# Optimization experiments

Hardware: AMD Instinct MI355X
Metric: run time of the kernel (lower is better)

The kernel has to match this reference:

```python
import jax, jax.numpy as jnp
import numpy as np

N_U = 100000; N_I = 100000; E = 500000
D_U = 256; D_I = 300; H = 128


def graph_conv(x_src, src, dst, n_src, n_dst, W, b, act):
    ones = jnp.ones(src.shape[0], dtype=x_src.dtype)
    deg_out = jnp.clip(jax.ops.segment_sum(ones, src, num_segments=n_src), 1.0)
    deg_in = jnp.clip(jax.ops.segment_sum(ones, dst, num_segments=n_dst), 1.0)
    h = (x_src * jax.lax.rsqrt(deg_out)[:, None]) @ W          # [n_src, H]
    m = jax.ops.segment_sum(h[src], dst, num_segments=n_dst)   # scatter-sum over edges
    m = m * jax.lax.rsqrt(deg_in)[:, None] + b
    return jax.nn.relu(m) if act else m


def setup_inputs():
    key = jax.random.key(0)
    ks = iter(jax.random.split(key, 64))
    f32 = jnp.float32
    inp = {}
    inp['feat_user'] = jax.random.normal(next(ks), (N_U, D_U), f32)
    inp['feat_item'] = jax.random.normal(next(ks), (N_I, D_I), f32)
    for et, (ns, nd) in [('uu', (N_U, N_U)), ('ui', (N_U, N_I)), ('iu', (N_I, N_U))]:
        inp[f'src_{et}'] = jax.random.randint(next(ks), (E,), 0, ns, dtype=jnp.int32)
        inp[f'dst_{et}'] = jax.random.randint(next(ks), (E,), 0, nd, dtype=jnp.int32)
    # HeteroLinear params
    inp['We_u'] = jax.random.normal(next(ks), (D_U, H), f32) * 0.02
    inp['be_u'] = jax.random.normal(next(ks), (H,), f32) * 0.02
    inp['We_i'] = jax.random.normal(next(ks), (D_I, H), f32) * 0.02
    inp['be_i'] = jax.random.normal(next(ks), (H,), f32) * 0.02
    # per-layer per-etype GraphConv params (3 layers x 3 etypes)
    for l in range(3):
        for et in ['uu', 'ui', 'iu']:
            inp[f'W{l}_{et}'] = jax.random.normal(next(ks), (H, H), f32) * 0.02
            inp[f'b{l}_{et}'] = jax.random.normal(next(ks), (H,), f32) * 0.02
    return inp


def reference(feat_user, feat_item, src_uu, dst_uu, src_ui, dst_ui, src_iu, dst_iu,
              We_u, be_u, We_i, be_i,
              W0_uu, b0_uu, W0_ui, b0_ui, W0_iu, b0_iu,
              W1_uu, b1_uu, W1_ui, b1_ui, W1_iu, b1_iu,
              W2_uu, b2_uu, W2_ui, b2_ui, W2_iu, b2_iu):
    # HeteroLinear embed
    hu = feat_user @ We_u + be_u
    hi = feat_item @ We_i + be_i
    # layer 0 (relu inside each GraphConv, then sum-aggregate per dst ntype)
    hu2 = graph_conv(hu, src_uu, dst_uu, N_U, N_U, W0_uu, b0_uu, True) \
        + graph_conv(hi, src_iu, dst_iu, N_I, N_U, W0_iu, b0_iu, True)
    hi2 = graph_conv(hu, src_ui, dst_ui, N_U, N_I, W0_ui, b0_ui, True)
    hu, hi = hu2, hi2
    # layer 1 (hidden)
    hu2 = graph_conv(hu, src_uu, dst_uu, N_U, N_U, W1_uu, b1_uu, True) \
        + graph_conv(hi, src_iu, dst_iu, N_I, N_U, W1_iu, b1_iu, True)
    hi2 = graph_conv(hu, src_ui, dst_ui, N_U, N_I, W1_ui, b1_ui, True)
    hu, hi = hu2, hi2
    # layer 2 (no activation)
    hu2 = graph_conv(hu, src_uu, dst_uu, N_U, N_U, W2_uu, b2_uu, False) \
        + graph_conv(hi, src_iu, dst_iu, N_I, N_U, W2_iu, b2_iu, False)
    hi2 = graph_conv(hu, src_ui, dst_ui, N_U, N_I, W2_ui, b2_ui, False)
    return hu2, hi2
```

## Files before the change

kernel.cpp:

```cpp
#include <hip/hip_runtime.h>

#define NU 100000
#define NI 100000
#define NE 500000
#define HD 128

using bf16x8 = __attribute__((ext_vector_type(8))) __bf16;
using f32x4  = __attribute__((ext_vector_type(4))) float;

__global__ __launch_bounds__(256) void src_count(
    const int* __restrict__ s0, const int* __restrict__ s1,
    const int* __restrict__ s2, float* __restrict__ deg)
{
    long long t = (long long)blockIdx.x * 256 + threadIdx.x;
    if (t >= 3LL * NE) return;
    int a = (int)(t / NE);
    int e = (int)(t - (long long)a * NE);
    const int* p = (a == 0) ? s0 : (a == 1) ? s1 : s2;
    atomicAdd(&deg[a * 200000 + p[e]], 1.0f);
}

__global__ __launch_bounds__(256) void deg_finalize(float* __restrict__ deg)
{
    int t = blockIdx.x * 256 + threadIdx.x;
    if (t < 600000) deg[t] = rsqrtf(fmaxf(deg[t], 1.0f));
}

__global__ __launch_bounds__(256) void rs_from_cnt(const int* __restrict__ cnt,
                                                   float* __restrict__ rs, int n)
{
    int t = blockIdx.x * 256 + threadIdx.x;
    if (t < n) rs[t] = rsqrtf(fmaxf((float)cnt[t], 1.0f));
}

__global__ __launch_bounds__(256) void count_dst(const int* __restrict__ dst,
                                                 int* __restrict__ cnt)
{
    int e = blockIdx.x * 256 + threadIdx.x;
    if (e < NE) atomicAdd(&cnt[dst[e]], 1);
}

__global__ __launch_bounds__(256) void scan_block(const int* __restrict__ cnt, int n,
                                                  int* __restrict__ rp,
                                                  int* __restrict__ bsum)
{
    __shared__ int s[256];
    int gid = blockIdx.x * 256 + threadIdx.x;
    int v = (gid < n) ? cnt[gid] : 0;
    s[threadIdx.x] = v;
    __syncthreads();
#pragma unroll
    for (int off = 1; off < 256; off <<= 1) {
        int t = (threadIdx.x >= off) ? s[threadIdx.x - off] : 0;
        __syncthreads();
        s[threadIdx.x] += t;
        __syncthreads();
    }
    if (gid < n) rp[gid] = s[threadIdx.x] - v;
    if (threadIdx.x == 255) bsum[blockIdx.x] = s[255];
}

__global__ __launch_bounds__(512) void scan_bsums(int* __restrict__ bsum, int nb)
{
    __shared__ int s[512];
    int v = (threadIdx.x < nb) ? bsum[threadIdx.x] : 0;
    s[threadIdx.x] = v;
    __syncthreads();
#pragma unroll
    for (int off = 1; off < 512; off <<= 1) {
        int t = (threadIdx.x >= off) ? s[threadIdx.x - off] : 0;
        __syncthreads();
        s[threadIdx.x] += t;
        __syncthreads();
    }
    if (threadIdx.x < nb) bsum[threadIdx.x] = s[threadIdx.x] - v;
    if (threadIdx.x == 0) bsum[nb] = s[nb - 1];
}

__global__ __launch_bounds__(256) void scan_add(int* __restrict__ rp,
                                                const int* __restrict__ bsum,
                                                int n, int nb)
{
    int gid = blockIdx.x * 256 + threadIdx.x;
    if (gid < n) rp[gid] += bsum[blockIdx.x];
    if (gid == 0) rp[n] = bsum[nb];
}

__global__ __launch_bounds__(256) void csr_fill(const int* __restrict__ src,
                                                const int* __restrict__ dst,
                                                const int* __restrict__ rp,
                                                int* __restrict__ cursor,
                                                int* __restrict__ eidx)
{
    int e = blockIdx.x * 256 + threadIdx.x;
    if (e >= NE) return;
    int d = dst[e];
    int pos = rp[d] + atomicAdd(&cursor[d], 1);
    eidx[pos] = src[e];
}

__global__ __launch_bounds__(256) void gather_scaled(
    const float* __restrict__ x, const float* __restrict__ rs,
    const int* __restrict__ rp, const int* __restrict__ eidx,
    float* __restrict__ m, int n)
{
    int row = blockIdx.x * 8 + (threadIdx.x >> 5);
    int c = (threadIdx.x & 31) * 4;
    if (row >= n) return;
    int beg = rp[row], end = rp[row + 1];
    float ax = 0.f, ay = 0.f, az = 0.f, aw = 0.f;
    for (int p = beg; p < end; ++p) {
        int s = eidx[p];
        float sc = rs[s];
        float4 v = *(const float4*)(x + (long long)s * HD + c);
        ax = fmaf(v.x, sc, ax);
        ay = fmaf(v.y, sc, ay);
        az = fmaf(v.z, sc, az);
        aw = fmaf(v.w, sc, aw);
    }
    *(float4*)(m + (long long)row * HD + c) = make_float4(ax, ay, az, aw);
}

__global__ __launch_bounds__(256) void convert_w(
    const float* __restrict__ W, int K, int Kpad,
    __bf16* __restrict__ Wh, __bf16* __restrict__ Wl)
{
    int t = blockIdx.x * 256 + threadIdx.x;
    if (t >= 128 * Kpad) return;
    int k = t >> 7;
    int n = t & 127;
    float x = (k < K) ? W[k * 128 + n] : 0.f;
    __bf16 h = (__bf16)x;
    float r = x - (float)h;
    Wh[n * Kpad + k] = h;
    Wl[n * Kpad + k] = (__bf16)r;
}

__global__ __launch_bounds__(256) void gemm128_mfma(
    const float* __restrict__ A, int K, int Kpad, int M,
    const __bf16* __restrict__ Wh, const __bf16* __restrict__ Wl,
    const float* __restrict__ bias,
    const float* __restrict__ out_scale,
    int do_relu, int do_accum,
    float* __restrict__ C)
{
    __shared__ __bf16 sAh[64 * 40];
    __shared__ __bf16 sAl[64 * 40];
    __shared__ __bf16 sWh[128 * 40];
    __shared__ __bf16 sWl[128 * 40];

    const int tid  = threadIdx.x;
    const int row0 = blockIdx.x * 64;
    const int lane = tid & 63;
    const int wv   = tid >> 6;
    const int lr   = lane & 15;
    const int lq   = lane >> 4;

    f32x4 acc[4][2];
#pragma unroll
    for (int i = 0; i < 4; ++i)
#pragma unroll
        for (int j = 0; j < 2; ++j)
#pragma unroll
            for (int t = 0; t < 4; ++t) acc[i][j][t] = 0.f;

    const int arow  = tid >> 2;
    const int akoff = (tid & 3) << 3;
    const int wcol  = tid >> 1;
    const int wkoff = (tid & 1) << 4;

    const int nk = Kpad >> 5;
    for (int kc = 0; kc < nk; ++kc) {
        const int k0 = kc << 5;
        {
            int row = row0 + arow;
            int k = k0 + akoff;
            float f[8];
            if (row < M && k + 7 < K) {
                float4 v0 = *(const float4*)(A + (long long)row * K + k);
                float4 v1 = *(const float4*)(A + (long long)row * K + k + 4);
                f[0] = v0.x; f[1] = v0.y; f[2] = v0.z; f[3] = v0.w;
                f[4] = v1.x; f[5] = v1.y; f[6] = v1.z; f[7] = v1.w;
            } else {
#pragma unroll
                for (int t = 0; t < 8; ++t)
                    f[t] = (row < M && k + t < K) ? A[(long long)row * K + k + t] : 0.f;
            }
            bf16x8 h8, l8;
#pragma unroll
            for (int t = 0; t < 8; ++t) {
                __bf16 h = (__bf16)f[t];
                h8[t] = h;
                l8[t] = (__bf16)(f[t] - (float)h);
            }
            *(bf16x8*)(&sAh[arow * 40 + akoff]) = h8;
            *(bf16x8*)(&sAl[arow * 40 + akoff]) = l8;
        }
        {
            const __bf16* ph = Wh + (long long)wcol * Kpad + k0 + wkoff;
            const __bf16* pl = Wl + (long long)wcol * Kpad + k0 + wkoff;
            bf16x8 w0 = *(const bf16x8*)(ph);
            bf16x8 w1 = *(const bf16x8*)(ph + 8);
            bf16x8 x0 = *(const bf16x8*)(pl);
            bf16x8 x1 = *(const bf16x8*)(pl + 8);
            *(bf16x8*)(&sWh[wcol * 40 + wkoff])     = w0;
            *(bf16x8*)(&sWh[wcol * 40 + wkoff + 8]) = w1;
            *(bf16x8*)(&sWl[wcol * 40 + wkoff])     = x0;
            *(bf16x8*)(&sWl[wcol * 40 + wkoff + 8]) = x1;
        }
        __syncthreads();
        bf16x8 bh[2], bl[2];
#pragma unroll
        for (int j = 0; j < 2; ++j) {
            int c = wv * 32 + j * 16 + lr;
            bh[j] = *(const bf16x8*)(&sWh[c * 40 + lq * 8]);
            bl[j] = *(const bf16x8*)(&sWl[c * 40 + lq * 8]);
        }
#pragma unroll
        for (int i = 0; i < 4; ++i) {
            bf16x8 ah = *(const bf16x8*)(&sAh[(i * 16 + lr) * 40 + lq * 8]);
            bf16x8 al = *(const bf16x8*)(&sAl[(i * 16 + lr) * 40 + lq * 8]);
#pragma unroll
            for (int j = 0; j < 2; ++j) {
                acc[i][j] = __builtin_amdgcn_mfma_f32_16x16x32_bf16(ah, bh[j], acc[i][j], 0, 0, 0);
                acc[i][j] = __builtin_amdgcn_mfma_f32_16x16x32_bf16(ah, bl[j], acc[i][j], 0, 0, 0);
                acc[i][j] = __builtin_amdgcn_mfma_f32_16x16x32_bf16(al, bh[j], acc[i][j], 0, 0, 0);
            }
        }
        __syncthreads();
    }

#pragma unroll
    for (int j = 0; j < 2; ++j) {
        int col = wv * 32 + j * 16 + lr;
        float bv = bias ? bias[col] : 0.f;
#pragma unroll
        for (int i = 0; i < 4; ++i) {
            int r0 = row0 + i * 16 + lq * 4;
#pragma unroll
            for (int t = 0; t < 4; ++t) {
                int row = r0 + t;
                if (row < M) {
                    float s = out_scale ? out_scale[row] : 1.f;
                    float v = acc[i][j][t] * s + bv;
                    if (do_relu) v = fmaxf(v, 0.f);
                    float* cp = C + (long long)row * 128 + col;
                    if (do_accum) v += *cp;
                    *cp = v;
                }
            }
        }
    }
}

static inline void build_csr(const int* src, const int* dst, int n_dst,
                             int* cnt, int* rp, int* cursor, int* eidx,
                             int* bsum, float* rs_in, hipStream_t stream)
{
    const int nb = (n_dst + 255) / 256;
    hipMemsetAsync(cnt, 0, n_dst * sizeof(int), stream);
    count_dst<<<(NE + 255) / 256, 256, 0, stream>>>(dst, cnt);
    rs_from_cnt<<<nb, 256, 0, stream>>>(cnt, rs_in, n_dst);
    scan_block<<<nb, 256, 0, stream>>>(cnt, n_dst, rp, bsum);
    scan_bsums<<<1, 512, 0, stream>>>(bsum, nb);
    scan_add<<<nb, 256, 0, stream>>>(rp, bsum, n_dst, nb);
    hipMemsetAsync(cursor, 0, n_dst * sizeof(int), stream);
    csr_fill<<<(NE + 255) / 256, 256, 0, stream>>>(src, dst, rp, cursor, eidx);
}

extern "C" void kernel_launch(void* const* d_in, const int* in_sizes, int n_in,
                              void* d_out, int out_size, void* d_ws, size_t ws_size,
                              hipStream_t stream)
{
    const float* feat_user = (const float*)d_in[0];
    const float* feat_item = (const float*)d_in[1];
    const int* src_uu = (const int*)d_in[2];
    const int* dst_uu = (const int*)d_in[3];
    const int* src_ui = (const int*)d_in[4];
    const int* dst_ui = (const int*)d_in[5];
    const int* src_iu = (const int*)d_in[6];
    const int* dst_iu = (const int*)d_in[7];
    const float* We_u = (const float*)d_in[8];
    const float* be_u = (const float*)d_in[9];
    const float* We_i = (const float*)d_in[10];
    const float* be_i = (const float*)d_in[11];

    float* hu = (float*)d_out;
    float* hi = hu + (size_t)NU * HD;

    float* ws   = (float*)d_ws;
    float* m_uu = ws;
    float* m_ui = m_uu + (size_t)NU * HD;
    float* m_iu = m_ui + (size_t)NI * HD;
    float* deg  = m_iu + (size_t)NU * HD;
    float* rs_out_uu = deg + 0;
    float* rs_in_uu  = deg + 100000;
    float* rs_out_ui = deg + 200000;
    float* rs_in_ui  = deg + 300000;
    float* rs_out_iu = deg + 400000;
    float* rs_in_iu  = deg + 500000;

    int* ib = (int*)(deg + 600000);
    int* rp_uu   = ib;                 ib += 100001;
    int* rp_ui   = ib;                 ib += 100001;
    int* rp_iu   = ib;                 ib += 100001;
    int* ei_uu   = ib;                 ib += NE;
    int* ei_ui   = ib;                 ib += NE;
    int* ei_iu   = ib;                 ib += NE;
    int* cnt     = ib;                 ib += 100000;
    int* cursor  = ib;                 ib += 100000;
    int* bsum    = ib;                 ib += 1024;

    uintptr_t wp = ((uintptr_t)ib + 63) & ~(uintptr_t)63;
    __bf16* wtbuf = (__bf16*)wp;
    __bf16* eu_h = wtbuf;
    __bf16* eu_l = eu_h + 128 * 256;
    __bf16* ei_h = eu_l + 128 * 256;
    __bf16* ei_l = ei_h + 128 * 320;
    __bf16* lw   = ei_l + 128 * 320;

    convert_w<<<(128 * 256 + 255) / 256, 256, 0, stream>>>(We_u, 256, 256, eu_h, eu_l);
    convert_w<<<(128 * 320 + 255) / 256, 256, 0, stream>>>(We_i, 300, 320, ei_h, ei_l);
    for (int l = 0; l < 3; ++l)
        for (int e = 0; e < 3; ++e) {
            const float* W = (const float*)d_in[12 + 6 * l + 2 * e];
            __bf16* h = lw + (size_t)(l * 3 + e) * 2 * 16384;
            convert_w<<<64, 256, 0, stream>>>(W, 128, 128, h, h + 16384);
        }

    hipMemsetAsync(deg, 0, 600000 * sizeof(float), stream);
    src_count<<<(3 * NE + 255) / 256, 256, 0, stream>>>(src_uu, src_ui, src_iu, deg);
    deg_finalize<<<(600000 + 255) / 256, 256, 0, stream>>>(deg);

    build_csr(src_uu, dst_uu, NU, cnt, rp_uu, cursor, ei_uu, bsum, rs_in_uu, stream);
    build_csr(src_ui, dst_ui, NI, cnt, rp_ui, cursor, ei_ui, bsum, rs_in_ui, stream);
    build_csr(src_iu, dst_iu, NU, cnt, rp_iu, cursor, ei_iu, bsum, rs_in_iu, stream);

    gemm128_mfma<<<(NU + 63) / 64, 256, 0, stream>>>(feat_user, 256, 256, NU,
                                                     eu_h, eu_l, be_u, nullptr, 0, 0, hu);
    gemm128_mfma<<<(NI + 63) / 64, 256, 0, stream>>>(feat_item, 300, 320, NI,
                                                     ei_h, ei_l, be_i, nullptr, 0, 0, hi);

    const int gat_blocks_u = (NU + 7) / 8;
    const int gat_blocks_i = (NI + 7) / 8;
    const int gemm_blocks_u = (NU + 63) / 64;
    const int gemm_blocks_i = (NI + 63) / 64;
    for (int l = 0; l < 3; ++l) {
        const float* b_uu = (const float*)d_in[12 + 6 * l + 1];
        const float* b_ui = (const float*)d_in[12 + 6 * l + 3];
        const float* b_iu = (const float*)d_in[12 + 6 * l + 5];
        __bf16* wh_uu = lw + (size_t)(l * 3 + 0) * 2 * 16384;
        __bf16* wh_ui = lw + (size_t)(l * 3 + 1) * 2 * 16384;
        __bf16* wh_iu = lw + (size_t)(l * 3 + 2) * 2 * 16384;
        const int relu = (l < 2) ? 1 : 0;

        gather_scaled<<<gat_blocks_u, 256, 0, stream>>>(hu, rs_out_uu, rp_uu, ei_uu, m_uu, NU);
        gather_scaled<<<gat_blocks_i, 256, 0, stream>>>(hu, rs_out_ui, rp_ui, ei_ui, m_ui, NI);
        gather_scaled<<<gat_blocks_u, 256, 0, stream>>>(hi, rs_out_iu, rp_iu, ei_iu, m_iu, NU);
        gemm128_mfma<<<gemm_blocks_u, 256, 0, stream>>>(m_uu, HD, HD, NU,
            wh_uu, wh_uu + 16384, b_uu, rs_in_uu, relu, 0, hu);
        gemm128_mfma<<<gemm_blocks_u, 256, 0, stream>>>(m_iu, HD, HD, NU,
            wh_iu, wh_iu + 16384, b_iu, rs_in_iu, relu, 1, hu);
        gemm128_mfma<<<gemm_blocks_i, 256, 0, stream>>>(m_ui, HD, HD, NI,
            wh_ui, wh_ui + 16384, b_ui, rs_in_ui, relu, 0, hi);
    }
}
```

Before: 1.523 ms.

## Add K=128 GEMM with register-resident weights and double-buffered A; unroll gather

Adds a specialised GEMM for the per-layer 128x128 transforms. Each wave keeps its bf16 hi/lo weight fragments in registers, and each block walks several 32-row chunks, double-buffering the converted A tiles in shared memory. This removes the per-tile weight reload and the K-loop staging of the generic kernel, at the cost of more registers and lower grid parallelism. Separately, the gather loop is unrolled by four so more independent row loads are in flight per thread.

Result: no change. 1.526 ms (+0.2%).

```diff
diff --git a/kernel.cpp b/kernel.cpp
--- a/kernel.cpp
+++ b/kernel.cpp
@@ -109,14 +109,29 @@
     if (row >= n) return;
     int beg = rp[row], end = rp[row + 1];
     float ax = 0.f, ay = 0.f, az = 0.f, aw = 0.f;
-    for (int p = beg; p < end; ++p) {
+    int p = beg;
+    for (; p + 4 <= end; p += 4) {
+        int s0 = eidx[p], s1 = eidx[p + 1], s2 = eidx[p + 2], s3 = eidx[p + 3];
+        float r0 = rs[s0], r1 = rs[s1], r2 = rs[s2], r3 = rs[s3];
+        float4 v0 = *(const float4*)(x + (long long)s0 * HD + c);
+        float4 v1 = *(const float4*)(x + (long long)s1 * HD + c);
+        float4 v2 = *(const float4*)(x + (long long)s2 * HD + c);
+        float4 v3 = *(const float4*)(x + (long long)s3 * HD + c);
+        ax = fmaf(v0.x, r0, ax); ay = fmaf(v0.y, r0, ay);
+        az = fmaf(v0.z, r0, az); aw = fmaf(v0.w, r0, aw);
+        ax = fmaf(v1.x, r1, ax); ay = fmaf(v1.y, r1, ay);
+        az = fmaf(v1.z, r1, az); aw = fmaf(v1.w, r1, aw);
+        ax = fmaf(v2.x, r2, ax); ay = fmaf(v2.y, r2, ay);
+        az = fmaf(v2.z, r2, az); aw = fmaf(v2.w, r2, aw);
+        ax = fmaf(v3.x, r3, ax); ay = fmaf(v3.y, r3, ay);
+        az = fmaf(v3.z, r3, az); aw = fmaf(v3.w, r3, aw);
+    }
+    for (; p < end; ++p) {
         int s = eidx[p];
         float sc = rs[s];
         float4 v = *(const float4*)(x + (long long)s * HD + c);
-        ax = fmaf(v.x, sc, ax);
-        ay = fmaf(v.y, sc, ay);
-        az = fmaf(v.z, sc, az);
-        aw = fmaf(v.w, sc, aw);
+        ax = fmaf(v.x, sc, ax); ay = fmaf(v.y, sc, ay);
+        az = fmaf(v.z, sc, az); aw = fmaf(v.w, sc, aw);
     }
     *(float4*)(m + (long long)row * HD + c) = make_float4(ax, ay, az, aw);
 }
@@ -134,6 +149,142 @@
     float r = x - (float)h;
     Wh[n * Kpad + k] = h;
     Wl[n * Kpad + k] = (__bf16)r;
+}
+
+#define CPB 3
+__global__ __launch_bounds__(256) void gemm_k128(
+    const float* __restrict__ A, int M,
+    const __bf16* __restrict__ Wh, const __bf16* __restrict__ Wl,
+    const float* __restrict__ bias,
+    const float* __restrict__ out_scale,
+    int do_relu, int do_accum,
+    float* __restrict__ C)
+{
+    __shared__ __bf16 sAh[2][32 * 136];
+    __shared__ __bf16 sAl[2][32 * 136];
+
+    const int tid  = threadIdx.x;
+    const int lane = tid & 63;
+    const int wv   = tid >> 6;
+    const int lr   = lane & 15;
+    const int lq   = lane >> 4;
+
+    bf16x8 bh[2][4], bl[2][4];
+#pragma unroll
+    for (int j = 0; j < 2; ++j)
+#pragma unroll
+        for (int kc = 0; kc < 4; ++kc) {
+            int col = wv * 32 + j * 16 + lr;
+            int k = kc * 32 + lq * 8;
+            bh[j][kc] = *(const bf16x8*)(Wh + col * 128 + k);
+            bl[j][kc] = *(const bf16x8*)(Wl + col * 128 + k);
+        }
+
+    const int nch = (M + 31) >> 5;
+    const int c0 = blockIdx.x * CPB;
+    const int cend = (c0 + CPB < nch) ? c0 + CPB : nch;
+
+    const int srow  = tid >> 3;
+    const int skoff = (tid & 7) << 4;
+
+    float4 pre[4];
+
+#define LOADREG(c)                                                              \
+    {                                                                           \
+        int row = (c) * 32 + srow;                                              \
+        if (row < M) {                                                          \
+            const float* p = A + (long long)row * 128 + skoff;                  \
+            pre[0] = *(const float4*)(p);                                       \
+            pre[1] = *(const float4*)(p + 4);                                   \
+            pre[2] = *(const float4*)(p + 8);                                   \
+            pre[3] = *(const float4*)(p + 12);                                  \
+        } else {                                                                \
+            pre[0] = pre[1] = pre[2] = pre[3] = make_float4(0.f, 0.f, 0.f, 0.f);\
+        }                                                                       \
+    }
+
+#define CVTWRITE(buf)                                                           \
+    {                                                                           \
+        float fv[16] = {pre[0].x, pre[0].y, pre[0].z, pre[0].w,                 \
+                        pre[1].x, pre[1].y, pre[1].z, pre[1].w,                 \
+                        pre[2].x, pre[2].y, pre[2].z, pre[2].w,                 \
+                        pre[3].x, pre[3].y, pre[3].z, pre[3].w};                \
+        bf16x8 h0, h1, l0, l1;                                                  \
+        _Pragma("unroll")                                                       \
+        for (int t = 0; t < 8; ++t) {                                           \
+            __bf16 h = (__bf16)fv[t];                                           \
+            h0[t] = h; l0[t] = (__bf16)(fv[t] - (float)h);                      \
+        }                                                                       \
+        _Pragma("unroll")                                                       \
+        for (int t = 0; t < 8; ++t) {                                           \
+            __bf16 h = (__bf16)fv[8 + t];                                       \
+            h1[t] = h; l1[t] = (__bf16)(fv[8 + t] - (float)h);                  \
+        }                                                                       \
+        *(bf16x8*)(&sAh[buf][srow * 136 + skoff])     = h0;                     \
+        *(bf16x8*)(&sAh[buf][srow * 136 + skoff + 8]) = h1;                     \
+        *(bf16x8*)(&sAl[buf][srow * 136 + skoff])     = l0;                     \
+        *(bf16x8*)(&sAl[buf][srow * 136 + skoff + 8]) = l1;                     \
+    }
+
+    LOADREG(c0);
+    CVTWRITE(0);
+    __syncthreads();
+
+    for (int c = c0; c < cend; ++c) {
+        const int buf = (c - c0) & 1;
+        const bool more = (c + 1 < cend);
+        if (more) LOADREG(c + 1);
+
+        f32x4 acc[2][2];
+#pragma unroll
+        for (int i = 0; i < 2; ++i)
+#pragma unroll
+            for (int j = 0; j < 2; ++j)
+#pragma unroll
+                for (int t = 0; t < 4; ++t) acc[i][j][t] = 0.f;
+
+#pragma unroll
+        for (int i = 0; i < 2; ++i) {
+#pragma unroll
+            for (int kc = 0; kc < 4; ++kc) {
+                bf16x8 ah = *(const bf16x8*)(&sAh[buf][(i * 16 + lr) * 136 + kc * 32 + lq * 8]);
+                bf16x8 al = *(const bf16x8*)(&sAl[buf][(i * 16 + lr) * 136 + kc * 32 + lq * 8]);
+#pragma unroll
+                for (int j = 0; j < 2; ++j) {
+                    acc[i][j] = __builtin_amdgcn_mfma_f32_16x16x32_bf16(ah, bh[j][kc], acc[i][j], 0, 0, 0);
+                    acc[i][j] = __builtin_amdgcn_mfma_f32_16x16x32_bf16(ah, bl[j][kc], acc[i][j], 0, 0, 0);
+                    acc[i][j] = __builtin_amdgcn_mfma_f32_16x16x32_bf16(al, bh[j][kc], acc[i][j], 0, 0, 0);
+                }
+            }
+        }
+
+#pragma unroll
+        for (int j = 0; j < 2; ++j) {
+            int col = wv * 32 + j * 16 + lr;
+            float bv = bias ? bias[col] : 0.f;
+#pragma unroll
+            for (int i = 0; i < 2; ++i) {
+                int r0 = c * 32 + i * 16 + lq * 4;
+#pragma unroll
+                for (int t = 0; t < 4; ++t) {
+                    int row = r0 + t;
+                    if (row < M) {
+                        float s = out_scale ? out_scale[row] : 1.f;
+                        float v = acc[i][j][t] * s + bv;
+                        if (do_relu) v = fmaxf(v, 0.f);
+                        float* cp = C + (long long)row * 128 + col;
+                        if (do_accum) v += *cp;
+                        *cp = v;
+                    }
+                }
+            }
+        }
+
+        if (more) CVTWRITE(buf ^ 1);
+        __syncthreads();
+    }
+#undef LOADREG
+#undef CVTWRITE
 }
 
 __global__ __launch_bounds__(256) void gemm128_mfma(
@@ -343,8 +494,10 @@
 
     const int gat_blocks_u = (NU + 7) / 8;
     const int gat_blocks_i = (NI + 7) / 8;
-    const int gemm_blocks_u = (NU + 63) / 64;
-    const int gemm_blocks_i = (NI + 63) / 64;
+    const int nch_u = (NU + 31) / 32;
+    const int nch_i = (NI + 31) / 32;
+    const int gk_blocks_u = (nch_u + CPB - 1) / CPB;
+    const int gk_blocks_i = (nch_i + CPB - 1) / CPB;
     for (int l = 0; l < 3; ++l) {
         const float* b_uu = (const float*)d_in[12 + 6 * l + 1];
         const float* b_ui = (const float*)d_in[12 + 6 * l + 3];
@@ -357,11 +510,11 @@
         gather_scaled<<<gat_blocks_u, 256, 0, stream>>>(hu, rs_out_uu, rp_uu, ei_uu, m_uu, NU);
         gather_scaled<<<gat_blocks_i, 256, 0, stream>>>(hu, rs_out_ui, rp_ui, ei_ui, m_ui, NI);
         gather_scaled<<<gat_blocks_u, 256, 0, stream>>>(hi, rs_out_iu, rp_iu, ei_iu, m_iu, NU);
-        gemm128_mfma<<<gemm_blocks_u, 256, 0, stream>>>(m_uu, HD, HD, NU,
+        gemm_k128<<<gk_blocks_u, 256, 0, stream>>>(m_uu, NU,
             wh_uu, wh_uu + 16384, b_uu, rs_in_uu, relu, 0, hu);
-        gemm128_mfma<<<gemm_blocks_u, 256, 0, stream>>>(m_iu, HD, HD, NU,
+        gemm_k128<<<gk_blocks_u, 256, 0, stream>>>(m_iu, NU,
             wh_iu, wh_iu + 16384, b_iu, rs_in_iu, relu, 1, hu);
-        gemm128_mfma<<<gemm_blocks_i, 256, 0, stream>>>(m_ui, HD, HD, NI,
+        gemm_k128<<<gk_blocks_i, 256, 0, stream>>>(m_ui, NI,
             wh_ui, wh_ui + 16384, b_ui, rs_in_ui, relu, 0, hi);
     }
 }
```

## Fuse neighbor gather with per-etype GEMM into one layer kernel

Applied to the files above, without the earlier changes.

Replaces the separate gather_scaled and gemm128_mfma launches in each layer with a single kernel. Each block gathers 32 destination rows straight into shared memory as hi/lo bf16 splits, then multiplies them by register-resident weight fragments using MFMA. The two user-side edge types are handled in the same block and summed in registers, which removes the full-size m_* intermediate buffers and the read-modify-write accumulate pass. Outputs ping-pong between workspace and output buffers so a layer never overwrites its own input. The trade-off is the gather's memory latency sitting in front of the MFMA work, with only 32 rows per block and no overlap between the two stages.

New measurement: 1.418 ms. -6.9%, faster.

```diff
diff --git a/kernel.cpp b/kernel.cpp
--- a/kernel.cpp
+++ b/kernel.cpp
@@ -97,28 +97,6 @@
     int d = dst[e];
     int pos = rp[d] + atomicAdd(&cursor[d], 1);
     eidx[pos] = src[e];
-}
-
-__global__ __launch_bounds__(256) void gather_scaled(
-    const float* __restrict__ x, const float* __restrict__ rs,
-    const int* __restrict__ rp, const int* __restrict__ eidx,
-    float* __restrict__ m, int n)
-{
-    int row = blockIdx.x * 8 + (threadIdx.x >> 5);
-    int c = (threadIdx.x & 31) * 4;
-    if (row >= n) return;
-    int beg = rp[row], end = rp[row + 1];
-    float ax = 0.f, ay = 0.f, az = 0.f, aw = 0.f;
-    for (int p = beg; p < end; ++p) {
-        int s = eidx[p];
-        float sc = rs[s];
-        float4 v = *(const float4*)(x + (long long)s * HD + c);
-        ax = fmaf(v.x, sc, ax);
-        ay = fmaf(v.y, sc, ay);
-        az = fmaf(v.z, sc, az);
-        aw = fmaf(v.w, sc, aw);
-    }
-    *(float4*)(m + (long long)row * HD + c) = make_float4(ax, ay, az, aw);
 }
 
 __global__ __launch_bounds__(256) void convert_w(
@@ -136,12 +114,174 @@
     Wl[n * Kpad + k] = (__bf16)r;
 }
 
+
+__device__ __forceinline__ void gather_stage(
+    const float* __restrict__ X, const int* __restrict__ rp,
+    const int* __restrict__ ei, const float* __restrict__ rs,
+    int r0, int M, int g, int gl, __bf16* sAh, __bf16* sAl)
+{
+#pragma unroll
+    for (int t = 0; t < 2; ++t) {
+        const int lrow = g * 2 + t;
+        const int row = r0 + lrow;
+        float a[8] = {0.f, 0.f, 0.f, 0.f, 0.f, 0.f, 0.f, 0.f};
+        if (row < M) {
+            int beg = rp[row], end = rp[row + 1];
+            int p = beg;
+            for (; p + 2 <= end; p += 2) {
+                int s0 = ei[p], s1 = ei[p + 1];
+                float w0 = rs[s0], w1 = rs[s1];
+                const float* x0 = X + (long long)s0 * HD + gl * 8;
+                const float* x1 = X + (long long)s1 * HD + gl * 8;
+                float4 u0 = *(const float4*)x0;
+                float4 u1 = *(const float4*)(x0 + 4);
+                float4 v0 = *(const float4*)x1;
+                float4 v1 = *(const float4*)(x1 + 4);
+                a[0] = fmaf(u0.x, w0, a[0]); a[1] = fmaf(u0.y, w0, a[1]);
+                a[2] = fmaf(u0.z, w0, a[2]); a[3] = fmaf(u0.w, w0, a[3]);
+                a[4] = fmaf(u1.x, w0, a[4]); a[5] = fmaf(u1.y, w0, a[5]);
+                a[6] = fmaf(u1.z, w0, a[6]); a[7] = fmaf(u1.w, w0, a[7]);
+                a[0] = fmaf(v0.x, w1, a[0]); a[1] = fmaf(v0.y, w1, a[1]);
+                a[2] = fmaf(v0.z, w1, a[2]); a[3] = fmaf(v0.w, w1, a[3]);
+                a[4] = fmaf(v1.x, w1, a[4]); a[5] = fmaf(v1.y, w1, a[5]);
+                a[6] = fmaf(v1.z, w1, a[6]); a[7] = fmaf(v1.w, w1, a[7]);
+            }
+            if (p < end) {
+                int s0 = ei[p];
+                float w0 = rs[s0];
+                const float* x0 = X + (long long)s0 * HD + gl * 8;
+                float4 u0 = *(const float4*)x0;
+                float4 u1 = *(const float4*)(x0 + 4);
+                a[0] = fmaf(u0.x, w0, a[0]); a[1] = fmaf(u0.y, w0, a[1]);
+                a[2] = fmaf(u0.z, w0, a[2]); a[3] = fmaf(u0.w, w0, a[3]);
+                a[4] = fmaf(u1.x, w0, a[4]); a[5] = fmaf(u1.y, w0, a[5]);
+                a[6] = fmaf(u1.z, w0, a[6]); a[7] = fmaf(u1.w, w0, a[7]);
+            }
+        }
+        bf16x8 h8, l8;
+#pragma unroll
+        for (int q = 0; q < 8; ++q) {
+            __bf16 hq = (__bf16)a[q];
+            h8[q] = hq;
+            l8[q] = (__bf16)(a[q] - (float)hq);
+        }
+        *(bf16x8*)(&sAh[lrow * 136 + gl * 8]) = h8;
+        *(bf16x8*)(&sAl[lrow * 136 + gl * 8]) = l8;
+    }
+}
+
+__device__ __forceinline__ void load_wfrags(const __bf16* __restrict__ W,
+                                            int wv, int lr, int lq,
+                                            bf16x8 bh[2][4], bf16x8 bl[2][4])
+{
+    const __bf16* Wlo = W + 16384;
+#pragma unroll
+    for (int j = 0; j < 2; ++j)
+#pragma unroll
+        for (int kc = 0; kc < 4; ++kc) {
+            int col = wv * 32 + j * 16 + lr;
+            int k = kc * 32 + lq * 8;
+            bh[j][kc] = *(const bf16x8*)(W + col * 128 + k);
+            bl[j][kc] = *(const bf16x8*)(Wlo + col * 128 + k);
+        }
+}
+
+__device__ __forceinline__ void mfma_tile(const __bf16* sAh, const __bf16* sAl,
+                                          int lr, int lq,
+                                          const bf16x8 bh[2][4], const bf16x8 bl[2][4],
+                                          f32x4 acc[2][2])
+{
+#pragma unroll
+    for (int i = 0; i < 2; ++i)
+#pragma unroll
+        for (int kc = 0; kc < 4; ++kc) {
+            bf16x8 ah = *(const bf16x8*)(&sAh[(i * 16 + lr) * 136 + kc * 32 + lq * 8]);
+            bf16x8 al = *(const bf16x8*)(&sAl[(i * 16 + lr) * 136 + kc * 32 + lq * 8]);
+#pragma unroll
+            for (int j = 0; j < 2; ++j) {
+                acc[i][j] = __builtin_amdgcn_mfma_f32_16x16x32_bf16(ah, bh[j][kc], acc[i][j], 0, 0, 0);
+                acc[i][j] = __builtin_amdgcn_mfma_f32_16x16x32_bf16(ah, bl[j][kc], acc[i][j], 0, 0, 0);
+                acc[i][j] = __builtin_amdgcn_mfma_f32_16x16x32_bf16(al, bh[j][kc], acc[i][j], 0, 0, 0);
+            }
+        }
+}
+
+__global__ __launch_bounds__(256) void layer_fused(
+    const float* __restrict__ Xa, const float* __restrict__ Xb,
+    const int* __restrict__ rp_a, const int* __restrict__ ei_a,
+    const float* __restrict__ rsa_s, const float* __restrict__ rsa_d,
+    const __bf16* __restrict__ Wa, const float* __restrict__ ba,
+    const int* __restrict__ rp_b, const int* __restrict__ ei_b,
+    const float* __restrict__ rsb_s, const float* __restrict__ rsb_d,
+    const __bf16* __restrict__ Wb, const float* __restrict__ bb,
+    int do_relu, int M, float* __restrict__ C)
+{
+    __shared__ __bf16 sAh[32 * 136];
+    __shared__ __bf16 sAl[32 * 136];
+
+    const int tid  = threadIdx.x;
+    const int lane = tid & 63;
+    const int wv   = tid >> 6;
+    const int lr   = lane & 15;
+    const int lq   = lane >> 4;
+    const int g    = tid >> 4;
+    const int gl   = tid & 15;
+    const int r0   = blockIdx.x * 32;
+    const bool dual = (Xb != nullptr);
+
+    bf16x8 bh[2][4], bl[2][4];
+    f32x4 accA[2][2], accB[2][2];
+#pragma unroll
+    for (int i = 0; i < 2; ++i)
+#pragma unroll
+        for (int j = 0; j < 2; ++j)
+#pragma unroll
+            for (int t = 0; t < 4; ++t) { accA[i][j][t] = 0.f; accB[i][j][t] = 0.f; }
+
+    load_wfrags(Wa, wv, lr, lq, bh, bl);
+    gather_stage(Xa, rp_a, ei_a, rsa_s, r0, M, g, gl, sAh, sAl);
+    __syncthreads();
+    mfma_tile(sAh, sAl, lr, lq, bh, bl, accA);
+
+    if (dual) {
+        __syncthreads();
+        load_wfrags(Wb, wv, lr, lq, bh, bl);
+        gather_stage(Xb, rp_b, ei_b, rsb_s, r0, M, g, gl, sAh, sAl);
+        __syncthreads();
+        mfma_tile(sAh, sAl, lr, lq, bh, bl, accB);
+    }
+
+#pragma unroll
+    for (int j = 0; j < 2; ++j) {
+        const int col = wv * 32 + j * 16 + lr;
+        const float bva = ba[col];
+        const float bvb = dual ? bb[col] : 0.f;
+#pragma unroll
+        for (int i = 0; i < 2; ++i) {
+            const int rbase = r0 + i * 16 + lq * 4;
+#pragma unroll
+            for (int t = 0; t < 4; ++t) {
+                const int row = rbase + t;
+                if (row < M) {
+                    float ya = accA[i][j][t] * rsa_d[row] + bva;
+                    if (do_relu) ya = fmaxf(ya, 0.f);
+                    float out = ya;
+                    if (dual) {
+                        float yb = accB[i][j][t] * rsb_d[row] + bvb;
+                        if (do_relu) yb = fmaxf(yb, 0.f);
+                        out += yb;
+                    }
+                    C[(long long)row * HD + col] = out;
+                }
+            }
+        }
+    }
+}
+
 __global__ __launch_bounds__(256) void gemm128_mfma(
     const float* __restrict__ A, int K, int Kpad, int M,
     const __bf16* __restrict__ Wh, const __bf16* __restrict__ Wl,
     const float* __restrict__ bias,
-    const float* __restrict__ out_scale,
-    int do_relu, int do_accum,
     float* __restrict__ C)
 {
     __shared__ __bf16 sAh[64 * 40];
@@ -241,12 +381,8 @@
             for (int t = 0; t < 4; ++t) {
                 int row = r0 + t;
                 if (row < M) {
-                    float s = out_scale ? out_scale[row] : 1.f;
-                    float v = acc[i][j][t] * s + bv;
-                    if (do_relu) v = fmaxf(v, 0.f);
-                    float* cp = C + (long long)row * 128 + col;
-                    if (do_accum) v += *cp;
-                    *cp = v;
+                    float v = acc[i][j][t] + bv;
+                    C[(long long)row * 128 + col] = v;
                 }
             }
         }
@@ -288,11 +424,10 @@
     float* hu = (float*)d_out;
     float* hi = hu + (size_t)NU * HD;
 
-    float* ws   = (float*)d_ws;
-    float* m_uu = ws;
-    float* m_ui = m_uu + (size_t)NU * HD;
-    float* m_iu = m_ui + (size_t)NI * HD;
-    float* deg  = m_iu + (size_t)NU * HD;
+    float* ws = (float*)d_ws;
+    float* wu = ws;
+    float* wi = wu + (size_t)NU * HD;
+    float* deg = wi + (size_t)NI * HD;
     float* rs_out_uu = deg + 0;
     float* rs_in_uu  = deg + 100000;
     float* rs_out_ui = deg + 200000;
@@ -337,31 +472,36 @@
     build_csr(src_iu, dst_iu, NU, cnt, rp_iu, cursor, ei_iu, bsum, rs_in_iu, stream);
 
     gemm128_mfma<<<(NU + 63) / 64, 256, 0, stream>>>(feat_user, 256, 256, NU,
-                                                     eu_h, eu_l, be_u, nullptr, 0, 0, hu);
+                                                     eu_h, eu_l, be_u, wu);
     gemm128_mfma<<<(NI + 63) / 64, 256, 0, stream>>>(feat_item, 300, 320, NI,
-                                                     ei_h, ei_l, be_i, nullptr, 0, 0, hi);
-
-    const int gat_blocks_u = (NU + 7) / 8;
-    const int gat_blocks_i = (NI + 7) / 8;
-    const int gemm_blocks_u = (NU + 63) / 64;
-    const int gemm_blocks_i = (NI + 63) / 64;
+                                                     ei_h, ei_l, be_i, wi);
+
+    const float* cu = wu; const float* ci = wi;
+    float* nu = hu; float* ni = hi;
+    const int blocks_u = (NU + 31) / 32;
+    const int blocks_i = (NI + 31) / 32;
     for (int l = 0; l < 3; ++l) {
         const float* b_uu = (const float*)d_in[12 + 6 * l + 1];
         const float* b_ui = (const float*)d_in[12 + 6 * l + 3];
         const float* b_iu = (const float*)d_in[12 + 6 * l + 5];
-        __bf16* wh_uu = lw + (size_t)(l * 3 + 0) * 2 * 16384;
-        __bf16* wh_ui = lw + (size_t)(l * 3 + 1) * 2 * 16384;
-        __bf16* wh_iu = lw + (size_t)(l * 3 + 2) * 2 * 16384;
+        const __bf16* Wuu = lw + (size_t)(l * 3 + 0) * 2 * 16384;
+        const __bf16* Wui = lw + (size_t)(l * 3 + 1) * 2 * 16384;
+        const __bf16* Wiu = lw + (size_t)(l * 3 + 2) * 2 * 16384;
         const int relu = (l < 2) ? 1 : 0;
 
-        gather_scaled<<<gat_blocks_u, 256, 0, stream>>>(hu, rs_out_uu, rp_uu, ei_uu, m_uu, NU);
-        gather_scaled<<<gat_blocks_i, 256, 0, stream>>>(hu, rs_out_ui, rp_ui, ei_ui, m_ui, NI);
-        gather_scaled<<<gat_blocks_u, 256, 0, stream>>>(hi, rs_out_iu, rp_iu, ei_iu, m_iu, NU);
-        gemm128_mfma<<<gemm_blocks_u, 256, 0, stream>>>(m_uu, HD, HD, NU,
-            wh_uu, wh_uu + 16384, b_uu, rs_in_uu, relu, 0, hu);
-        gemm128_mfma<<<gemm_blocks_u, 256, 0, stream>>>(m_iu, HD, HD, NU,
-            wh_iu, wh_iu + 16384, b_iu, rs_in_iu, relu, 1, hu);
-        gemm128_mfma<<<gemm_blocks_i, 256, 0, stream>>>(m_ui, HD, HD, NI,
-            wh_ui, wh_ui + 16384, b_ui, rs_in_ui, relu, 0, hi);
-    }
-}
+        layer_fused<<<blocks_u, 256, 0, stream>>>(
+            cu, ci,
+            rp_uu, ei_uu, rs_out_uu, rs_in_uu, Wuu, b_uu,
+            rp_iu, ei_iu, rs_out_iu, rs_in_iu, Wiu, b_iu,
+            relu, NU, nu);
+        layer_fused<<<blocks_i, 256, 0, stream>>>(
+            cu, nullptr,
+            rp_ui, ei_ui, rs_out_ui, rs_in_ui, Wui, b_ui,
+            rp_ui, ei_ui, rs_out_ui, rs_in_ui, Wui, b_ui,
+            relu, NI, ni);
+
+        const float* tu = cu; const float* ti = ci;
+        cu = nu; ci = ni;
+        nu = (float*)tu; ni = (float*)ti;
+    }
+}
```
